# Optimization experiments

Hardware: AMD Instinct MI355X
Metric: run time of the kernel (lower is better)

Reference implementation:

```python
import jax, jax.numpy as jnp
import numpy as np
from jax import lax

MARGIN_1 = 0.3
ALPHA_1 = 0.5
B, D = 256, 512
N_CLASSES = 32


def setup_inputs() -> dict:
    key = jax.random.key(0)
    k1, k2, k3 = jax.random.split(key, 3)
    feature = jax.random.normal(k1, (B, D), dtype=jnp.float32)
    sub = jax.random.randint(k2, (B,), 0, 2, dtype=jnp.int64)
    targets = jax.random.randint(k3, (B,), 0, N_CLASSES, dtype=jnp.int64)
    return {"feature": feature, "sub": sub, "targets": targets}


def _masked_softmax(logits, mask):
    # softmax over last axis restricted to `mask`; rows with empty mask -> all zeros
    # (matches torch behavior where an empty gather yields a zero transition matrix)
    neg = jnp.where(mask, logits, -jnp.inf)
    m = jnp.max(neg, axis=-1, keepdims=True)
    m = jnp.where(jnp.isfinite(m), m, 0.0)
    e = jnp.where(mask, jnp.exp(logits - m), 0.0)
    s = jnp.sum(e, axis=-1, keepdims=True)
    return e / jnp.maximum(s, 1e-30)


def _masked_mean(v, m):
    cnt = jnp.maximum(jnp.sum(m), 1).astype(v.dtype)
    return jnp.sum(jnp.where(m, v, 0.0)) / cnt


def _transition_loss(feature, sub, targets, margin_1, alpha_1):
    n = feature.shape[0]
    sim = feature @ feature.T  # [B,B], reused for every anchor

    def trans(mask_r, mask_c):
        # ab: rows -> mask_c columns; ba: rows -> mask_r columns.
        # Columns outside the mask are exactly 0, so the matmul only mixes
        # the same subset entries as torch's gathered mm, embedded in [B,B].
        ab = _masked_softmax(sim, mask_c[None, :])  # [B,B]
        ba = _masked_softmax(sim, mask_r[None, :])  # [B,B]
        tr = ab @ ba  # valid on rows/cols in mask_r
        return jnp.sqrt(jnp.clip(tr, 1e-12))

    def body(acc, i):
        is_pos = targets == targets[i]  # includes i itself
        is_neg = ~is_pos
        intra = sub == sub[i]
        cross = ~intra
        mpi = is_pos & intra
        mpc = is_pos & cross
        mni = is_neg & intra
        mnc = is_neg & cross
        trans_pos = trans(mpi, mpc)
        trans_neg = trans(mni, mnc)
        loss_ap = _masked_mean(jnp.clip(trans_neg + (margin_1 - alpha_1), 0.0),
                               mni[:, None] & mni[None, :])
        loss_an = _masked_mean(jnp.clip(alpha_1 - trans_pos, 0.0),
                               mpi[:, None] & mpi[None, :])
        return acc + loss_ap + loss_an, None

    total, _ = lax.scan(body, jnp.float32(0.0), jnp.arange(n))
    return total / n


def reference(feature, sub, targets):
    # NB: the torch module computes normalize(feature) into `x` but never uses it;
    # the loss consumes the raw `feature`, so we do the same.
    return _transition_loss(feature, sub, targets, MARGIN_1, ALPHA_1)
```

## Files before the change

kernel.cpp:

```cpp
#include <hip/hip_runtime.h>
#include <hip/hip_bf16.h>
#include <math.h>


constexpr int kB = 256;
constexpr int kD = 512;
constexpr float NEG_BIG = -3.4e38f;

typedef _Float16 f16x8 __attribute__((ext_vector_type(8)));
typedef float f32x16 __attribute__((ext_vector_type(16)));

constexpr int O_SIM   = 0;
constexpr int O_M     = 262144;
constexpr int O_L     = 327680;
constexpr int O_IDX   = 393216;
constexpr int O_CNT   = 524288;
constexpr int O_METAI = 525312;
constexpr int O_METAS = 527360;
constexpr int O_E     = 527872;
constexpr int O_F     = 658944;
constexpr int O_PART  = 790016;
constexpr int O_X     = 822784;
constexpr int XSTRIDE = 256 * 264;

__global__ __launch_bounds__(256)
void simKernel(const float* __restrict__ f, float* __restrict__ sim) {
  __shared__ float As[16][68];
  __shared__ float Bs[16][68];
  const int tid = threadIdx.x;
  const int tx = tid & 15, ty = tid >> 4;
  const int lr = tid >> 4, lc4 = (tid & 15) * 4;
  const int rowBase = blockIdx.y * 16, colBase = blockIdx.x * 16;
  float a0 = 0.f, a1 = 0.f, a2 = 0.f, a3 = 0.f;
  for (int k0 = 0; k0 < kD; k0 += 64) {
    float4 va = *(const float4*)&f[(rowBase + lr) * kD + k0 + lc4];
    float4 vb = *(const float4*)&f[(colBase + lr) * kD + k0 + lc4];
    *(float4*)&As[lr][lc4] = va;
    *(float4*)&Bs[lr][lc4] = vb;
    __syncthreads();
#pragma unroll
    for (int kk = 0; kk < 64; kk += 16) {
      float4 x0 = *(const float4*)&As[ty][kk];
      float4 y0 = *(const float4*)&Bs[tx][kk];
      a0 = fmaf(x0.x, y0.x, a0); a0 = fmaf(x0.y, y0.y, a0);
      a0 = fmaf(x0.z, y0.z, a0); a0 = fmaf(x0.w, y0.w, a0);
      float4 x1 = *(const float4*)&As[ty][kk + 4];
      float4 y1 = *(const float4*)&Bs[tx][kk + 4];
      a1 = fmaf(x1.x, y1.x, a1); a1 = fmaf(x1.y, y1.y, a1);
      a1 = fmaf(x1.z, y1.z, a1); a1 = fmaf(x1.w, y1.w, a1);
      float4 x2 = *(const float4*)&As[ty][kk + 8];
      float4 y2 = *(const float4*)&Bs[tx][kk + 8];
      a2 = fmaf(x2.x, y2.x, a2); a2 = fmaf(x2.y, y2.y, a2);
      a2 = fmaf(x2.z, y2.z, a2); a2 = fmaf(x2.w, y2.w, a2);
      float4 x3 = *(const float4*)&As[ty][kk + 12];
      float4 y3 = *(const float4*)&Bs[tx][kk + 12];
      a3 = fmaf(x3.x, y3.x, a3); a3 = fmaf(x3.y, y3.y, a3);
      a3 = fmaf(x3.z, y3.z, a3); a3 = fmaf(x3.w, y3.w, a3);
    }
    __syncthreads();
  }
  sim[(rowBase + ty) * kB + colBase + tx] = (a0 + a1) + (a2 + a3);
}

__global__ __launch_bounds__(64)
void listKernel(const int* __restrict__ tgt, const int* __restrict__ sub,
                unsigned short* __restrict__ idxAll, int* __restrict__ cnt4,
                int4* __restrict__ metaI, float* __restrict__ metaS) {
  const int p = blockIdx.x, t = p >> 1, s = p & 1;
  const int lane = threadIdx.x;
  __shared__ unsigned char cat[256];
  __shared__ int cnts[4];
  for (int chunk = 0; chunk < 4; chunk++) {
    int c = chunk * 64 + lane;
    bool pos = (tgt[c] == t), intra = (sub[c] == s);
    cat[c] = (unsigned char)(pos ? (intra ? 0 : 1) : (intra ? 2 : 3));
  }
  __syncthreads();
  for (int l = 0; l < 4; l++) {
    int base = 0;
    for (int chunk = 0; chunk < 4; chunk++) {
      int c = chunk * 64 + lane;
      bool fl = (cat[c] == (unsigned char)l);
      unsigned long long mm = __ballot(fl);
      if (fl) {
        int pfx = __popcll(mm & ((1ull << lane) - 1ull));
        idxAll[(p * 4 + l) * 256 + base + pfx] = (unsigned short)c;
      }
      base += __popcll(mm);
    }
    if (lane == 0) cnts[l] = base;
  }
  __syncthreads();
  if (lane == 0) {
    cnt4[p * 4 + 0] = cnts[0]; cnt4[p * 4 + 1] = cnts[1];
    cnt4[p * 4 + 2] = cnts[2]; cnt4[p * 4 + 3] = cnts[3];
    const int mult = cnts[0];
#pragma unroll
    for (int part = 0; part < 2; part++) {
      int nR = part ? cnts[0] : cnts[2];
      int nK = part ? cnts[1] : cnts[3];
      int KP = (nK + 15) & ~15;
      int4 mi; mi.x = nR; mi.y = nK; mi.z = KP + 8; mi.w = KP;
      metaI[p * 2 + part] = mi;
      metaS[p * 2 + part] = (mult > 0 && nR > 0 && nK > 0)
                              ? (float)mult / ((float)nR * (float)nR) : 0.f;
    }
  }
}

__global__ __launch_bounds__(512)
void statsKernel(const float* __restrict__ sim, const int* __restrict__ tgt,
                 const int* __restrict__ sub, float* __restrict__ Mv,
                 float* __restrict__ Lv) {
  const int a = blockIdx.x;
  const int lane = threadIdx.x & 63, wave = threadIdx.x >> 6;
  const float4 v4 = ((const float4*)(sim + a * kB))[lane];
  const int4 t4 = ((const int4*)tgt)[lane];
  const int4 s4 = ((const int4*)sub)[lane];
  const int ta = tgt[a], sa = sub[a];
  for (int jj = 0; jj < 8; jj++) {
    const int p = wave * 8 + jj, t = p >> 1, s = p & 1;
    const bool pa = (ta == t), ia = (sa == s);
    const bool e0 = ((t4.x == t) == pa) && ((s4.x == s) != ia);
    const bool e1 = ((t4.y == t) == pa) && ((s4.y == s) != ia);
    const bool e2 = ((t4.z == t) == pa) && ((s4.z == s) != ia);
    const bool e3 = ((t4.w == t) == pa) && ((s4.w == s) != ia);
    float m = fmaxf(fmaxf(e0 ? v4.x : NEG_BIG, e1 ? v4.y : NEG_BIG),
                    fmaxf(e2 ? v4.z : NEG_BIG, e3 ? v4.w : NEG_BIG));
#pragma unroll
    for (int o = 32; o >= 1; o >>= 1) m = fmaxf(m, __shfl_xor(m, o, 64));
    float ss = (e0 ? __expf(v4.x - m) : 0.f) + (e1 ? __expf(v4.y - m) : 0.f)
             + (e2 ? __expf(v4.z - m) : 0.f) + (e3 ? __expf(v4.w - m) : 0.f);
#pragma unroll
    for (int o = 32; o >= 1; o >>= 1) ss += __shfl_xor(ss, o, 64);
    if (lane == 0) { Mv[p * 256 + a] = m; Lv[p * 256 + a] = __logf(ss); }
  }
}

__global__ __launch_bounds__(512)
void buildXKernel(const float* __restrict__ sim, const float* __restrict__ Mv,
                  const float* __restrict__ Lv, const unsigned short* __restrict__ idxAll,
                  const int4* __restrict__ metaI, const float* __restrict__ metaS,
                  _Float16* __restrict__ X, float* __restrict__ E, float* __restrict__ F) {
  const int b = blockIdx.x, pp = b >> 2, slice = b & 3;
  const int p = pp >> 1, part = pp & 1;
  if (metaS[pp] == 0.f) return;
  const int4 mi = metaI[pp];
  const int nR = mi.x, nK = mi.y, SKh = mi.z, KP = mi.w;
  const unsigned short* iR = idxAll + (p * 4 + (part ? 0 : 2)) * 256;
  const unsigned short* iK = idxAll + (p * 4 + (part ? 1 : 3)) * 256;
  __shared__ float qs[256];
  __shared__ unsigned short iks[256];
  const int tid = threadIdx.x, lane = tid & 63, wave = tid >> 6;
  if (tid < 256) {
    int ik = (tid < nK) ? (int)iK[tid] : 0;
    iks[tid] = (unsigned short)ik;
    qs[tid] = (tid < nK) ? 0.5f * (Mv[p * 256 + ik] + Lv[p * 256 + ik]) : 0.f;
  }
  __syncthreads();
  _Float16* Xp = X + pp * XSTRIDE;
  for (int r = slice * 8 + wave; r < nR; r += 32) {
    const int a = (int)iR[r];
    const float* srow = sim + a * kB;
    float vals[4];
    float w = NEG_BIG;
#pragma unroll
    for (int j = 0; j < 4; j++) {
      int k = lane + 64 * j;
      float v = NEG_BIG;
      if (k < nK) v = srow[(int)iks[k]] - qs[k];
      vals[j] = v;
      w = fmaxf(w, v);
    }
#pragma unroll
    for (int o = 32; o >= 1; o >>= 1) w = fmaxf(w, __shfl_xor(w, o, 64));
#pragma unroll
    for (int j = 0; j < 4; j++) {
      int k = lane + 64 * j;
      if (k < KP) Xp[r * SKh + k] = (_Float16)__expf(vals[j] - w);
    }
    if (lane == 0) {
      float u = Mv[p * 256 + a] + Lv[p * 256 + a];
      E[pp * 256 + r] = __expf(0.5f * (w - u));
      F[pp * 256 + r] = __expf(0.5f * w);
    }
  }
}

__global__ __launch_bounds__(256)
void gramKernel(const _Float16* __restrict__ X, const float* __restrict__ E,
                const float* __restrict__ F, const int4* __restrict__ metaI,
                const float* __restrict__ metaS, float* __restrict__ partials) {
  const int lane = threadIdx.x & 63, wave = threadIdx.x >> 6;
  const int job = blockIdx.x * 4 + wave;
  const int pp = job >> 6, tile = job & 63;
  const int4 mi = metaI[pp];
  const int nR = mi.x, SKh = mi.z, KP = mi.w;
  const int r0 = (tile >> 3) << 5, c0 = (tile & 7) << 5;
  const float scale = metaS[pp];
  float res = 0.f;
  if (scale != 0.f && r0 < nR && c0 < nR) {
    const _Float16* Xp = X + pp * XSTRIDE;
    const int l31 = lane & 31, kg = lane >> 5;
    const _Float16* pa = Xp + (r0 + l31) * SKh + 8 * kg;
    const _Float16* pb = Xp + (c0 + l31) * SKh + 8 * kg;
    f32x16 acc;
#pragma unroll
    for (int g = 0; g < 16; g++) acc[g] = 0.f;
    for (int kb = 0; kb < KP; kb += 16) {
      f16x8 av = *(const f16x8*)(pa + kb);
      f16x8 bv = *(const f16x8*)(pb + kb);
      acc = __builtin_amdgcn_mfma_f32_32x32x16_f16(av, bv, acc, 0, 0, 0);
    }
    const int c = c0 + l31;
    if (c < nR) {
      const float Fc = F[pp * 256 + c];
      const int rb = r0 + 4 * kg;
      const bool neg = ((pp & 1) == 0);
#pragma unroll
      for (int g = 0; g < 16; g++) {
        const int r = rb + (g & 3) + ((g >> 2) << 3);
        if (r < nR) {
          float x = E[pp * 256 + r] * Fc * sqrtf(acc[g]);
          x = fmaxf(x, 1e-6f);
          res += neg ? fmaxf(x - 0.2f, 0.f) : fmaxf(0.5f - x, 0.f);
        }
      }
    }
  }
#pragma unroll
  for (int o = 32; o >= 1; o >>= 1) res += __shfl_xor(res, o, 64);
  if (lane == 0) partials[job] = res * scale;
}

__global__ __launch_bounds__(1024)
void finalKernel(const float* __restrict__ partials, const int* __restrict__ cnt4,
                 float* __restrict__ out) {
  const int tid = threadIdx.x;
  float s = 0.f;
#pragma unroll
  for (int j = 0; j < 8; j++) s += partials[tid + 1024 * j];
  if (tid < 64) {
    int c0 = cnt4[tid * 4 + 0], c1 = cnt4[tid * 4 + 1];
    if (c0 > 0 && c1 == 0) s += (float)c0 * (0.5f - 1e-6f);
  }
#pragma unroll
  for (int o = 32; o >= 1; o >>= 1) s += __shfl_xor(s, o, 64);
  __shared__ float red[16];
  if ((tid & 63) == 0) red[tid >> 6] = s;
  __syncthreads();
  if (tid == 0) {
    float t = 0.f;
    for (int w = 0; w < 16; w++) t += red[w];
    out[0] = t * (1.0f / 256.0f);
  }
}

extern "C" void kernel_launch(void* const* d_in, const int* in_sizes, int n_in,
                              void* d_out, int out_size, void* d_ws, size_t ws_size,
                              hipStream_t stream) {
  (void)in_sizes; (void)n_in; (void)out_size; (void)ws_size;
  const float* feature = (const float*)d_in[0];
  const int* subv = (const int*)d_in[1];
  const int* tgtv = (const int*)d_in[2];
  float* out = (float*)d_out;
  char* ws = (char*)d_ws;

  float* sim = (float*)(ws + O_SIM);
  float* Mv = (float*)(ws + O_M);
  float* Lv = (float*)(ws + O_L);
  unsigned short* idxAll = (unsigned short*)(ws + O_IDX);
  int* cnt4 = (int*)(ws + O_CNT);
  int4* metaI = (int4*)(ws + O_METAI);
  float* metaS = (float*)(ws + O_METAS);
  float* E = (float*)(ws + O_E);
  float* F = (float*)(ws + O_F);
  float* partials = (float*)(ws + O_PART);
  _Float16* X = (_Float16*)(ws + O_X);

  simKernel<<<dim3(16, 16), 256, 0, stream>>>(feature, sim);
  listKernel<<<64, 64, 0, stream>>>(tgtv, subv, idxAll, cnt4, metaI, metaS);
  statsKernel<<<256, 512, 0, stream>>>(sim, tgtv, subv, Mv, Lv);
  buildXKernel<<<512, 512, 0, stream>>>(sim, Mv, Lv, idxAll, metaI, metaS, X, E, F);
  gramKernel<<<2048, 256, 0, stream>>>(X, E, F, metaI, metaS, partials);
  finalKernel<<<1, 1024, 0, stream>>>(partials, cnt4, out);
}
```

Before: 107.0 us.

## Fuse six kernels into two, building the transition matrix in LDS

Cuts the pipeline from six launches to two. The first kernel fuses the similarity matmul, the per-row softmax statistics and the list building. The second kernel, one block per (class, sub, part), builds the fp16 X matrix directly in LDS and runs the MFMA Gram reduction there, then accumulates into the output with atomicAdd. This removes the global round trips for X, E, F and partials and the launch overhead of the extra kernels. In exchange only 128 blocks run the pair work, each needing about 145 KB of dynamic LDS, so parallelism is much lower. The sim matmul is now a naive per-thread dot product reading from global memory, and the float atomic accumulation order is nondeterministic.

```diff
diff --git a/kernel.cpp b/kernel.cpp
--- a/kernel.cpp
+++ b/kernel.cpp
@@ -10,200 +10,206 @@
 typedef _Float16 f16x8 __attribute__((ext_vector_type(8)));
 typedef float f32x16 __attribute__((ext_vector_type(16)));
 
-constexpr int O_SIM   = 0;
-constexpr int O_M     = 262144;
-constexpr int O_L     = 327680;
-constexpr int O_IDX   = 393216;
-constexpr int O_CNT   = 524288;
-constexpr int O_METAI = 525312;
-constexpr int O_METAS = 527360;
-constexpr int O_E     = 527872;
-constexpr int O_F     = 658944;
-constexpr int O_PART  = 790016;
-constexpr int O_X     = 822784;
-constexpr int XSTRIDE = 256 * 264;
-
-__global__ __launch_bounds__(256)
-void simKernel(const float* __restrict__ f, float* __restrict__ sim) {
-  __shared__ float As[16][68];
-  __shared__ float Bs[16][68];
-  const int tid = threadIdx.x;
-  const int tx = tid & 15, ty = tid >> 4;
-  const int lr = tid >> 4, lc4 = (tid & 15) * 4;
-  const int rowBase = blockIdx.y * 16, colBase = blockIdx.x * 16;
-  float a0 = 0.f, a1 = 0.f, a2 = 0.f, a3 = 0.f;
-  for (int k0 = 0; k0 < kD; k0 += 64) {
-    float4 va = *(const float4*)&f[(rowBase + lr) * kD + k0 + lc4];
-    float4 vb = *(const float4*)&f[(colBase + lr) * kD + k0 + lc4];
-    *(float4*)&As[lr][lc4] = va;
-    *(float4*)&Bs[lr][lc4] = vb;
-    __syncthreads();
-#pragma unroll
-    for (int kk = 0; kk < 64; kk += 16) {
-      float4 x0 = *(const float4*)&As[ty][kk];
-      float4 y0 = *(const float4*)&Bs[tx][kk];
-      a0 = fmaf(x0.x, y0.x, a0); a0 = fmaf(x0.y, y0.y, a0);
-      a0 = fmaf(x0.z, y0.z, a0); a0 = fmaf(x0.w, y0.w, a0);
-      float4 x1 = *(const float4*)&As[ty][kk + 4];
-      float4 y1 = *(const float4*)&Bs[tx][kk + 4];
-      a1 = fmaf(x1.x, y1.x, a1); a1 = fmaf(x1.y, y1.y, a1);
-      a1 = fmaf(x1.z, y1.z, a1); a1 = fmaf(x1.w, y1.w, a1);
-      float4 x2 = *(const float4*)&As[ty][kk + 8];
-      float4 y2 = *(const float4*)&Bs[tx][kk + 8];
-      a2 = fmaf(x2.x, y2.x, a2); a2 = fmaf(x2.y, y2.y, a2);
-      a2 = fmaf(x2.z, y2.z, a2); a2 = fmaf(x2.w, y2.w, a2);
-      float4 x3 = *(const float4*)&As[ty][kk + 12];
-      float4 y3 = *(const float4*)&Bs[tx][kk + 12];
-      a3 = fmaf(x3.x, y3.x, a3); a3 = fmaf(x3.y, y3.y, a3);
-      a3 = fmaf(x3.z, y3.z, a3); a3 = fmaf(x3.w, y3.w, a3);
-    }
-    __syncthreads();
-  }
-  sim[(rowBase + ty) * kB + colBase + tx] = (a0 + a1) + (a2 + a3);
-}
-
-__global__ __launch_bounds__(64)
-void listKernel(const int* __restrict__ tgt, const int* __restrict__ sub,
-                unsigned short* __restrict__ idxAll, int* __restrict__ cnt4,
-                int4* __restrict__ metaI, float* __restrict__ metaS) {
-  const int p = blockIdx.x, t = p >> 1, s = p & 1;
-  const int lane = threadIdx.x;
-  __shared__ unsigned char cat[256];
-  __shared__ int cnts[4];
-  for (int chunk = 0; chunk < 4; chunk++) {
-    int c = chunk * 64 + lane;
-    bool pos = (tgt[c] == t), intra = (sub[c] == s);
-    cat[c] = (unsigned char)(pos ? (intra ? 0 : 1) : (intra ? 2 : 3));
-  }
-  __syncthreads();
-  for (int l = 0; l < 4; l++) {
-    int base = 0;
+constexpr int O_SIM = 0;
+constexpr int O_M   = 262144;
+constexpr int O_L   = 327680;
+constexpr int O_IDX = 393216;
+constexpr int O_CNT = 524288;
+constexpr int O_MI  = 525312;
+constexpr int O_MS  = 527360;
+
+constexpr int XB_Q   = 135168;
+constexpr int XB_E   = XB_Q + 1024;
+constexpr int XB_F   = XB_E + 1024;
+constexpr int XB_IK  = XB_F + 1024;
+constexpr int XB_IR  = XB_IK + 512;
+constexpr int XB_ROW = XB_IR + 512;
+constexpr int XB_RED = XB_ROW + 8320;
+constexpr int K2_LDS = XB_RED + 32;
+
+__global__ __launch_bounds__(512)
+void simStatsKernel(const float* __restrict__ f, const int* __restrict__ tgt,
+                    const int* __restrict__ sub, float* __restrict__ sim,
+                    float* __restrict__ Mv, float* __restrict__ Lv,
+                    unsigned short* __restrict__ idxAll, int* __restrict__ cnt4,
+                    int4* __restrict__ metaI, float* __restrict__ metaS,
+                    float* __restrict__ out) {
+  __shared__ float frow[2][512];
+  __shared__ float panel[2][260];
+  const int tid = threadIdx.x, lane = tid & 63, wave = tid >> 6;
+  const int r0 = blockIdx.x * 2;
+  if (tid < 256)
+    ((float4*)frow)[tid] = ((const float4*)(f + (size_t)r0 * kD))[tid];
+  __syncthreads();
+  {
+    const int col = tid & 255, rh = tid >> 8;
+    const float* fc = f + (size_t)col * kD;
+    const float* fr = frow[rh];
+    float acc = 0.f;
+#pragma unroll 8
+    for (int k = 0; k < kD; k += 4) {
+      float4 b = *(const float4*)(fc + k);
+      float4 a = *(const float4*)(fr + k);
+      acc = fmaf(a.x, b.x, acc); acc = fmaf(a.y, b.y, acc);
+      acc = fmaf(a.z, b.z, acc); acc = fmaf(a.w, b.w, acc);
+    }
+    sim[(size_t)(r0 + rh) * kB + col] = acc;
+    panel[rh][col] = acc;
+  }
+  __syncthreads();
+  {
+    const int row = wave & 1, a = r0 + row;
+    const float4 v4 = ((const float4*)panel[row])[lane];
+    const int4 t4 = ((const int4*)tgt)[lane];
+    const int4 s4 = ((const int4*)sub)[lane];
+    const int ta = tgt[a], sa = sub[a];
+    const int p0 = (wave >> 1) * 16;
+    for (int jj = 0; jj < 16; jj++) {
+      const int p = p0 + jj, t = p >> 1, s = p & 1;
+      const bool pa = (ta == t), ia = (sa == s);
+      const bool e0 = ((t4.x == t) == pa) && ((s4.x == s) != ia);
+      const bool e1 = ((t4.y == t) == pa) && ((s4.y == s) != ia);
+      const bool e2 = ((t4.z == t) == pa) && ((s4.z == s) != ia);
+      const bool e3 = ((t4.w == t) == pa) && ((s4.w == s) != ia);
+      float m = fmaxf(fmaxf(e0 ? v4.x : NEG_BIG, e1 ? v4.y : NEG_BIG),
+                      fmaxf(e2 ? v4.z : NEG_BIG, e3 ? v4.w : NEG_BIG));
+#pragma unroll
+      for (int o = 32; o >= 1; o >>= 1) m = fmaxf(m, __shfl_xor(m, o, 64));
+      float ss = (e0 ? __expf(v4.x - m) : 0.f) + (e1 ? __expf(v4.y - m) : 0.f)
+               + (e2 ? __expf(v4.z - m) : 0.f) + (e3 ? __expf(v4.w - m) : 0.f);
+#pragma unroll
+      for (int o = 32; o >= 1; o >>= 1) ss += __shfl_xor(ss, o, 64);
+      if (lane == 0) { Mv[p * 256 + a] = m; Lv[p * 256 + a] = __logf(ss); }
+    }
+  }
+  if (blockIdx.x < 64 && wave == 0) {
+    const int p = blockIdx.x, t = p >> 1, s = p & 1;
+    int base[4] = {0, 0, 0, 0};
     for (int chunk = 0; chunk < 4; chunk++) {
       int c = chunk * 64 + lane;
-      bool fl = (cat[c] == (unsigned char)l);
-      unsigned long long mm = __ballot(fl);
-      if (fl) {
-        int pfx = __popcll(mm & ((1ull << lane) - 1ull));
-        idxAll[(p * 4 + l) * 256 + base + pfx] = (unsigned short)c;
-      }
-      base += __popcll(mm);
-    }
-    if (lane == 0) cnts[l] = base;
-  }
-  __syncthreads();
-  if (lane == 0) {
-    cnt4[p * 4 + 0] = cnts[0]; cnt4[p * 4 + 1] = cnts[1];
-    cnt4[p * 4 + 2] = cnts[2]; cnt4[p * 4 + 3] = cnts[3];
-    const int mult = cnts[0];
-#pragma unroll
-    for (int part = 0; part < 2; part++) {
-      int nR = part ? cnts[0] : cnts[2];
-      int nK = part ? cnts[1] : cnts[3];
-      int KP = (nK + 15) & ~15;
-      int4 mi; mi.x = nR; mi.y = nK; mi.z = KP + 8; mi.w = KP;
-      metaI[p * 2 + part] = mi;
-      metaS[p * 2 + part] = (mult > 0 && nR > 0 && nK > 0)
-                              ? (float)mult / ((float)nR * (float)nR) : 0.f;
-    }
-  }
+      bool pos = (tgt[c] == t), intra = (sub[c] == s);
+      int cat = pos ? (intra ? 0 : 1) : (intra ? 2 : 3);
+#pragma unroll
+      for (int l = 0; l < 4; l++) {
+        bool fl = (cat == l);
+        unsigned long long mm = __ballot(fl);
+        if (fl) {
+          int pf = __popcll(mm & ((1ull << lane) - 1ull));
+          idxAll[(p * 4 + l) * 256 + base[l] + pf] = (unsigned short)c;
+        }
+        base[l] += __popcll(mm);
+      }
+    }
+    if (lane == 0) {
+      cnt4[p * 4 + 0] = base[0]; cnt4[p * 4 + 1] = base[1];
+      cnt4[p * 4 + 2] = base[2]; cnt4[p * 4 + 3] = base[3];
+      const int mult = base[0];
+#pragma unroll
+      for (int part = 0; part < 2; part++) {
+        int nR = part ? base[0] : base[2];
+        int nK = part ? base[1] : base[3];
+        int KP = (nK + 15) & ~15;
+        int4 mi; mi.x = nR; mi.y = nK; mi.z = KP + 8; mi.w = KP;
+        metaI[p * 2 + part] = mi;
+        metaS[p * 2 + part] = (mult > 0 && nR > 0 && nK > 0)
+            ? (float)mult / ((float)nR * (float)nR * 256.f) : 0.f;
+      }
+    }
+  }
+  if (blockIdx.x == 64 && tid == 0) out[0] = 0.f;
 }
 
 __global__ __launch_bounds__(512)
-void statsKernel(const float* __restrict__ sim, const int* __restrict__ tgt,
-                 const int* __restrict__ sub, float* __restrict__ Mv,
-                 float* __restrict__ Lv) {
-  const int a = blockIdx.x;
-  const int lane = threadIdx.x & 63, wave = threadIdx.x >> 6;
-  const float4 v4 = ((const float4*)(sim + a * kB))[lane];
-  const int4 t4 = ((const int4*)tgt)[lane];
-  const int4 s4 = ((const int4*)sub)[lane];
-  const int ta = tgt[a], sa = sub[a];
-  for (int jj = 0; jj < 8; jj++) {
-    const int p = wave * 8 + jj, t = p >> 1, s = p & 1;
-    const bool pa = (ta == t), ia = (sa == s);
-    const bool e0 = ((t4.x == t) == pa) && ((s4.x == s) != ia);
-    const bool e1 = ((t4.y == t) == pa) && ((s4.y == s) != ia);
-    const bool e2 = ((t4.z == t) == pa) && ((s4.z == s) != ia);
-    const bool e3 = ((t4.w == t) == pa) && ((s4.w == s) != ia);
-    float m = fmaxf(fmaxf(e0 ? v4.x : NEG_BIG, e1 ? v4.y : NEG_BIG),
-                    fmaxf(e2 ? v4.z : NEG_BIG, e3 ? v4.w : NEG_BIG));
-#pragma unroll
-    for (int o = 32; o >= 1; o >>= 1) m = fmaxf(m, __shfl_xor(m, o, 64));
-    float ss = (e0 ? __expf(v4.x - m) : 0.f) + (e1 ? __expf(v4.y - m) : 0.f)
-             + (e2 ? __expf(v4.z - m) : 0.f) + (e3 ? __expf(v4.w - m) : 0.f);
-#pragma unroll
-    for (int o = 32; o >= 1; o >>= 1) ss += __shfl_xor(ss, o, 64);
-    if (lane == 0) { Mv[p * 256 + a] = m; Lv[p * 256 + a] = __logf(ss); }
-  }
-}
-
-__global__ __launch_bounds__(512)
-void buildXKernel(const float* __restrict__ sim, const float* __restrict__ Mv,
-                  const float* __restrict__ Lv, const unsigned short* __restrict__ idxAll,
-                  const int4* __restrict__ metaI, const float* __restrict__ metaS,
-                  _Float16* __restrict__ X, float* __restrict__ E, float* __restrict__ F) {
-  const int b = blockIdx.x, pp = b >> 2, slice = b & 3;
-  const int p = pp >> 1, part = pp & 1;
-  if (metaS[pp] == 0.f) return;
+void pairKernel(const float* __restrict__ sim, const float* __restrict__ Mv,
+                const float* __restrict__ Lv, const unsigned short* __restrict__ idxAll,
+                const int* __restrict__ cnt4, const int4* __restrict__ metaI,
+                const float* __restrict__ metaS, float* __restrict__ out) {
+  extern __shared__ char smemRaw[];
+  const int pp = blockIdx.x, p = pp >> 1, part = pp & 1;
+  const int tid = threadIdx.x, lane = tid & 63, wave = tid >> 6;
+  const float scale = metaS[pp];
+  if (scale == 0.f) {
+    if (part == 1 && tid == 0) {
+      int nR = cnt4[p * 4 + 0], nK = cnt4[p * 4 + 1];
+      if (nR > 0 && nK == 0)
+        atomicAdd(out, (float)nR * (0.5f - 1e-6f) * (1.f / 256.f));
+    }
+    return;
+  }
   const int4 mi = metaI[pp];
   const int nR = mi.x, nK = mi.y, SKh = mi.z, KP = mi.w;
-  const unsigned short* iR = idxAll + (p * 4 + (part ? 0 : 2)) * 256;
-  const unsigned short* iK = idxAll + (p * 4 + (part ? 1 : 3)) * 256;
-  __shared__ float qs[256];
-  __shared__ unsigned short iks[256];
-  const int tid = threadIdx.x, lane = tid & 63, wave = tid >> 6;
+  const int nT = (nR + 31) >> 5, nRp = nT << 5;
+
+  _Float16* Xh = (_Float16*)smemRaw;
+  float* q   = (float*)(smemRaw + XB_Q);
+  float* Ev  = (float*)(smemRaw + XB_E);
+  float* Fv  = (float*)(smemRaw + XB_F);
+  unsigned short* iKs = (unsigned short*)(smemRaw + XB_IK);
+  unsigned short* iRs = (unsigned short*)(smemRaw + XB_IR);
+  float* rowst = (float*)(smemRaw + XB_ROW);
+  float* wred  = (float*)(smemRaw + XB_RED);
+
+  const unsigned short* giR = idxAll + (p * 4 + (part ? 0 : 2)) * 256;
+  const unsigned short* giK = idxAll + (p * 4 + (part ? 1 : 3)) * 256;
   if (tid < 256) {
-    int ik = (tid < nK) ? (int)iK[tid] : 0;
-    iks[tid] = (unsigned short)ik;
-    qs[tid] = (tid < nK) ? 0.5f * (Mv[p * 256 + ik] + Lv[p * 256 + ik]) : 0.f;
-  }
-  __syncthreads();
-  _Float16* Xp = X + pp * XSTRIDE;
-  for (int r = slice * 8 + wave; r < nR; r += 32) {
-    const int a = (int)iR[r];
-    const float* srow = sim + a * kB;
-    float vals[4];
-    float w = NEG_BIG;
-#pragma unroll
-    for (int j = 0; j < 4; j++) {
-      int k = lane + 64 * j;
-      float v = NEG_BIG;
-      if (k < nK) v = srow[(int)iks[k]] - qs[k];
-      vals[j] = v;
-      w = fmaxf(w, v);
-    }
-#pragma unroll
-    for (int o = 32; o >= 1; o >>= 1) w = fmaxf(w, __shfl_xor(w, o, 64));
-#pragma unroll
-    for (int j = 0; j < 4; j++) {
-      int k = lane + 64 * j;
-      if (k < KP) Xp[r * SKh + k] = (_Float16)__expf(vals[j] - w);
-    }
-    if (lane == 0) {
-      float u = Mv[p * 256 + a] + Lv[p * 256 + a];
-      E[pp * 256 + r] = __expf(0.5f * (w - u));
-      F[pp * 256 + r] = __expf(0.5f * w);
-    }
-  }
-}
-
-__global__ __launch_bounds__(256)
-void gramKernel(const _Float16* __restrict__ X, const float* __restrict__ E,
-                const float* __restrict__ F, const int4* __restrict__ metaI,
-                const float* __restrict__ metaS, float* __restrict__ partials) {
-  const int lane = threadIdx.x & 63, wave = threadIdx.x >> 6;
-  const int job = blockIdx.x * 4 + wave;
-  const int pp = job >> 6, tile = job & 63;
-  const int4 mi = metaI[pp];
-  const int nR = mi.x, SKh = mi.z, KP = mi.w;
-  const int r0 = (tile >> 3) << 5, c0 = (tile & 7) << 5;
-  const float scale = metaS[pp];
+    iRs[tid] = (tid < nR) ? giR[tid] : (unsigned short)0;
+    int ik = (tid < nK) ? (int)giK[tid] : 0;
+    iKs[tid] = (unsigned short)ik;
+    q[tid] = (tid < nK) ? 0.5f * (Mv[p * 256 + ik] + Lv[p * 256 + ik]) : 0.f;
+  }
+  __syncthreads();
+
+  auto loadRow = [&](int r) -> float4 {
+    if (r < nR)
+      return ((const float4*)(sim + (size_t)iRs[r] * kB))[lane];
+    float4 z; z.x = z.y = z.z = z.w = 0.f; return z;
+  };
+  float4 v = loadRow(wave);
+  for (int r = wave; r < nRp; r += 8) {
+    float4 vn = loadRow(r + 8);
+    if (r < nR) {
+      *(float4*)(rowst + wave * 260 + lane * 4) = v;
+      asm volatile("s_waitcnt lgkmcnt(0)" ::: "memory");
+      float vals[4];
+      float w = NEG_BIG;
+#pragma unroll
+      for (int j = 0; j < 4; j++) {
+        int k = lane + 64 * j;
+        float x = NEG_BIG;
+        if (k < nK) x = rowst[wave * 260 + (int)iKs[k]] - q[k];
+        vals[j] = x; w = fmaxf(w, x);
+      }
+#pragma unroll
+      for (int o = 32; o >= 1; o >>= 1) w = fmaxf(w, __shfl_xor(w, o, 64));
+#pragma unroll
+      for (int j = 0; j < 4; j++) {
+        int k = lane + 64 * j;
+        if (k < KP) Xh[r * SKh + k] = (_Float16)__expf(vals[j] - w);
+      }
+      if (lane == 0) {
+        float u = Mv[p * 256 + (int)iRs[r]] + Lv[p * 256 + (int)iRs[r]];
+        Ev[r] = __expf(0.5f * (w - u));
+        Fv[r] = __expf(0.5f * w);
+      }
+    } else {
+#pragma unroll
+      for (int j = 0; j < 4; j++) {
+        int k = lane + 64 * j;
+        if (k < KP) Xh[r * SKh + k] = (_Float16)0.f;
+      }
+      if (lane == 0) { Ev[r] = 0.f; Fv[r] = 0.f; }
+    }
+    v = vn;
+  }
+  __syncthreads();
+
   float res = 0.f;
-  if (scale != 0.f && r0 < nR && c0 < nR) {
-    const _Float16* Xp = X + pp * XSTRIDE;
-    const int l31 = lane & 31, kg = lane >> 5;
-    const _Float16* pa = Xp + (r0 + l31) * SKh + 8 * kg;
-    const _Float16* pb = Xp + (c0 + l31) * SKh + 8 * kg;
+  const int l31 = lane & 31, kg = lane >> 5;
+  const int nTiles = nT * nT;
+  for (int t = wave; t < nTiles; t += 8) {
+    const int r0t = (t / nT) << 5, c0t = (t % nT) << 5;
+    const _Float16* pa = Xh + (r0t + l31) * SKh + 8 * kg;
+    const _Float16* pb = Xh + (c0t + l31) * SKh + 8 * kg;
     f32x16 acc;
 #pragma unroll
     for (int g = 0; g < 16; g++) acc[g] = 0.f;
@@ -212,47 +218,30 @@
       f16x8 bv = *(const f16x8*)(pb + kb);
       acc = __builtin_amdgcn_mfma_f32_32x32x16_f16(av, bv, acc, 0, 0, 0);
     }
-    const int c = c0 + l31;
+    const int c = c0t + l31;
     if (c < nR) {
-      const float Fc = F[pp * 256 + c];
-      const int rb = r0 + 4 * kg;
-      const bool neg = ((pp & 1) == 0);
+      const float Fc = Fv[c];
+      const int rb = r0t + 4 * kg;
 #pragma unroll
       for (int g = 0; g < 16; g++) {
         const int r = rb + (g & 3) + ((g >> 2) << 3);
         if (r < nR) {
-          float x = E[pp * 256 + r] * Fc * sqrtf(acc[g]);
+          float x = Ev[r] * Fc * sqrtf(acc[g]);
           x = fmaxf(x, 1e-6f);
-          res += neg ? fmaxf(x - 0.2f, 0.f) : fmaxf(0.5f - x, 0.f);
+          res += part ? fmaxf(0.5f - x, 0.f) : fmaxf(x - 0.2f, 0.f);
         }
       }
     }
   }
 #pragma unroll
   for (int o = 32; o >= 1; o >>= 1) res += __shfl_xor(res, o, 64);
-  if (lane == 0) partials[job] = res * scale;
-}
-
-__global__ __launch_bounds__(1024)
-void finalKernel(const float* __restrict__ partials, const int* __restrict__ cnt4,
-                 float* __restrict__ out) {
-  const int tid = threadIdx.x;
-  float s = 0.f;
-#pragma unroll
-  for (int j = 0; j < 8; j++) s += partials[tid + 1024 * j];
-  if (tid < 64) {
-    int c0 = cnt4[tid * 4 + 0], c1 = cnt4[tid * 4 + 1];
-    if (c0 > 0 && c1 == 0) s += (float)c0 * (0.5f - 1e-6f);
-  }
-#pragma unroll
-  for (int o = 32; o >= 1; o >>= 1) s += __shfl_xor(s, o, 64);
-  __shared__ float red[16];
-  if ((tid & 63) == 0) red[tid >> 6] = s;
+  if (lane == 0) wred[wave] = res;
   __syncthreads();
   if (tid == 0) {
-    float t = 0.f;
-    for (int w = 0; w < 16; w++) t += red[w];
-    out[0] = t * (1.0f / 256.0f);
+    float tot = 0.f;
+#pragma unroll
+    for (int w2 = 0; w2 < 8; w2++) tot += wred[w2];
+    atomicAdd(out, tot * scale);
   }
 }
 
@@ -271,17 +260,14 @@
   float* Lv = (float*)(ws + O_L);
   unsigned short* idxAll = (unsigned short*)(ws + O_IDX);
   int* cnt4 = (int*)(ws + O_CNT);
-  int4* metaI = (int4*)(ws + O_METAI);
-  float* metaS = (float*)(ws + O_METAS);
-  float* E = (float*)(ws + O_E);
-  float* F = (float*)(ws + O_F);
-  float* partials = (float*)(ws + O_PART);
-  _Float16* X = (_Float16*)(ws + O_X);
-
-  simKernel<<<dim3(16, 16), 256, 0, stream>>>(feature, sim);
-  listKernel<<<64, 64, 0, stream>>>(tgtv, subv, idxAll, cnt4, metaI, metaS);
-  statsKernel<<<256, 512, 0, stream>>>(sim, tgtv, subv, Mv, Lv);
-  buildXKernel<<<512, 512, 0, stream>>>(sim, Mv, Lv, idxAll, metaI, metaS, X, E, F);
-  gramKernel<<<2048, 256, 0, stream>>>(X, E, F, metaI, metaS, partials);
-  finalKernel<<<1, 1024, 0, stream>>>(partials, cnt4, out);
+  int4* metaI = (int4*)(ws + O_MI);
+  float* metaS = (float*)(ws + O_MS);
+
+  (void)hipFuncSetAttribute(reinterpret_cast<const void*>(pairKernel),
+                            hipFuncAttributeMaxDynamicSharedMemorySize, K2_LDS);
+
+  simStatsKernel<<<128, 512, 0, stream>>>(feature, tgtv, subv, sim, Mv, Lv,
+                                          idxAll, cnt4, metaI, metaS, out);
+  pairKernel<<<128, 512, K2_LDS, stream>>>(sim, Mv, Lv, idxAll, cnt4,
+                                           metaI, metaS, out);
 }
```

Measured after the change: 118.6 us. +10.9%, slower.
